# Performance work log

Measured on AMD Instinct MI355X. Metric: run time of the kernel, lower is better.

## Reference

```python
import jax, jax.numpy as jnp
import numpy as np

N_NODES = 100000
N_EDGES = 1600000
C_IN = 500
HIDDEN = 256
C_OUT = 50
K = 10
K_HALF = K // 2  # 5
ALPHA = 0.1


def _prop(x, src, dst, norm, n):
    # one propagate(): gather source features, scale by edge norm, scatter-add to dst
    msg = norm[:, None] * x[src]          # [E, F]
    return jax.ops.segment_sum(msg, dst, num_segments=n)


def setup_inputs() -> dict:
    key = jax.random.key(0)
    k0, k1, k2, k3 = jax.random.split(key, 4)
    x = jax.random.normal(k0, (N_NODES, C_IN), dtype=jnp.float32)
    edge_index = jax.random.randint(k1, (2, N_EDGES), 0, N_NODES, dtype=jnp.int32)
    # temp[k] = alpha * (1-alpha)^(2k), k = 0..K//2  (even-order PPR coefficients)
    temp = jnp.asarray(ALPHA * (1.0 - ALPHA) ** (2 * np.arange(K_HALF + 1)), dtype=jnp.float32)
    W1 = jax.random.normal(k2, (C_IN, HIDDEN), dtype=jnp.float32) / np.sqrt(C_IN).astype(np.float32)
    b1 = jnp.zeros((HIDDEN,), jnp.float32)
    W2 = jax.random.normal(k3, (HIDDEN, C_OUT), dtype=jnp.float32) / np.sqrt(HIDDEN).astype(np.float32)
    b2 = jnp.zeros((C_OUT,), jnp.float32)
    return {"x": x, "edge_index": edge_index, "W1": W1, "b1": b1, "W2": W2, "b2": b2, "temp": temp}


def reference(x, edge_index, W1, b1, W2, b2, temp):
    n = x.shape[0]
    src, dst = edge_index[0], edge_index[1]
    # sym-normalized adjacency A_hat = D^-1/2 A D^-1/2.
    # (get_laplacian 'sym' then add_self_loops(-norm, 1.0): the -1/+1 diagonal
    #  entries cancel under scatter-add, leaving exactly A_hat.)
    deg = jax.ops.segment_sum(jnp.ones_like(src, dtype=x.dtype), src, num_segments=n)
    dinv = jnp.where(deg > 0, jax.lax.rsqrt(jnp.maximum(deg, 1e-12)), 0.0)
    norm = dinv[src] * dinv[dst]          # [E]

    # MLP (dropout is identity in eval mode)
    h = jax.nn.relu(x @ W1 + b1)
    h = h @ W2 + b2                        # [N, C_OUT]

    hidden0 = h * temp[0]

    def body(k, carry):
        xk, hid = carry
        xk = _prop(xk, src, dst, norm, n)  # A_hat @ x
        xk = _prop(xk, src, dst, norm, n)  # A_hat^2 @ x
        hid = hid + temp[k + 1] * xk
        return (xk, hid)

    _, hidden = jax.lax.fori_loop(0, K_HALF, body, (h, hidden0))
    return jax.nn.log_softmax(hidden, axis=1)
```

## Files before the change

### kernel.cpp

```cpp
#include <hip/hip_runtime.h>

#define NN 100000
#define CIN 500
#define KPAD 512
#define HID 256
#define COUT 50
#define NPADOUT 64
#define FPAD 64

#define NBLK 256
#define CB 128
#define NC ((NN + CB - 1) / CB)
#define NCB (NC * NBLK)
#define NCB2 (2 * NCB)

typedef __attribute__((ext_vector_type(8))) short short8;
typedef __attribute__((ext_vector_type(4))) float f32x4;

static __device__ __forceinline__ unsigned short f2bf(float f) {
  union { float f; unsigned u; } v; v.f = f;
  unsigned r = (v.u + 0x7fffu + ((v.u >> 16) & 1u)) >> 16;
  return (unsigned short)r;
}


__launch_bounds__(256)
__global__ void k_p1(const int* __restrict__ src, const int* __restrict__ dst,
                     int* __restrict__ blk_cnt, int E, int chunk) {
  __shared__ int bd[NC], bs[NC];
  int tid = threadIdx.x;
  for (int i = tid; i < NC; i += 256) { bd[i] = 0; bs[i] = 0; }
  __syncthreads();
  int e0 = blockIdx.x * chunk, e1 = min(E, e0 + chunk);
  for (int e = e0 + tid; e < e1; e += 256) {
    atomicAdd(&bd[dst[e] >> 7], 1);
    atomicAdd(&bs[src[e] >> 7], 1);
  }
  __syncthreads();
  for (int i = tid; i < NC; i += 256) {
    blk_cnt[i * NBLK + blockIdx.x] = bd[i];
    blk_cnt[NCB + i * NBLK + blockIdx.x] = bs[i];
  }
}


__global__ void k_scan_a(const int* __restrict__ hist, int* __restrict__ incl,
                         int* __restrict__ bsum, int n) {
  __shared__ int ts[256];
  int tid = threadIdx.x;
  int base = blockIdx.x * 1024 + tid * 4;
  int a0 = 0, a1 = 0, a2 = 0, a3 = 0;
  if (base + 3 < n) {
    a0 = hist[base]; a1 = hist[base + 1]; a2 = hist[base + 2]; a3 = hist[base + 3];
  } else {
    if (base     < n) a0 = hist[base];
    if (base + 1 < n) a1 = hist[base + 1];
    if (base + 2 < n) a2 = hist[base + 2];
    if (base + 3 < n) a3 = hist[base + 3];
  }
  a1 += a0; a2 += a1; a3 += a2;
  ts[tid] = a3;
  __syncthreads();
  for (int o = 1; o < 256; o <<= 1) {
    int v = ts[tid];
    if (tid >= o) v += ts[tid - o];
    __syncthreads();
    ts[tid] = v;
    __syncthreads();
  }
  int ex = tid ? ts[tid - 1] : 0;
  if (base     < n) incl[base]     = a0 + ex;
  if (base + 1 < n) incl[base + 1] = a1 + ex;
  if (base + 2 < n) incl[base + 2] = a2 + ex;
  if (base + 3 < n) incl[base + 3] = a3 + ex;
  if (tid == 255) bsum[blockIdx.x] = ts[255];
}

__global__ void k_scan_b(const int* __restrict__ bsum, int* __restrict__ bpre, int nb) {
  __shared__ int s[512];
  int tid = threadIdx.x;
  s[tid] = (tid < nb) ? bsum[tid] : 0;
  __syncthreads();
  for (int o = 1; o < 512; o <<= 1) {
    int v = s[tid];
    if (tid >= o) v += s[tid - o];
    __syncthreads();
    s[tid] = v;
    __syncthreads();
  }
  if (tid < nb) bpre[tid] = tid ? s[tid - 1] : 0;
}

__global__ void k_scan_c(const int* __restrict__ incl, const int* __restrict__ bpre,
                         int* __restrict__ slot, int n) {
  int g = blockIdx.x * 256 + threadIdx.x;
  if (g < n) {
    slot[g + 1] = incl[g] + bpre[g >> 10];
    if (g == 0) slot[0] = 0;
  }
}


__launch_bounds__(256)
__global__ void k_p2(const int* __restrict__ src, const int* __restrict__ dst,
                     const int* __restrict__ slot, int* __restrict__ pkd,
                     unsigned char* __restrict__ pks, int E, int chunk) {
  __shared__ int cd[NC], cs[NC];
  int tid = threadIdx.x;
  for (int i = tid; i < NC; i += 256) {
    cd[i] = slot[i * NBLK + blockIdx.x];
    cs[i] = slot[NCB + i * NBLK + blockIdx.x] - E;
  }
  __syncthreads();
  int e0 = blockIdx.x * chunk, e1 = min(E, e0 + chunk);
  for (int e = e0 + tid; e < e1; e += 256) {
    int s = src[e], d = dst[e];
    int pd = atomicAdd(&cd[d >> 7], 1);
    pkd[pd] = (s << 7) | (d & 127);
    int ps = atomicAdd(&cs[s >> 7], 1);
    pks[ps] = (unsigned char)(s & 127);
  }
}


__launch_bounds__(256)
__global__ void k_p3s(const int* __restrict__ slot, const unsigned char* __restrict__ pks,
                      float* __restrict__ dinv, int E) {
  __shared__ int hist[CB];
  int b = blockIdx.x, tid = threadIdx.x;
  if (tid < CB) hist[tid] = 0;
  __syncthreads();
  int s0 = slot[NCB + b * NBLK] - E;
  int s1 = slot[NCB + (b + 1) * NBLK] - E;
  for (int e = s0 + tid; e < s1; e += 256) atomicAdd(&hist[pks[e]], 1);
  __syncthreads();
  if (tid < CB) {
    int node = b * CB + tid;
    if (node < NN) {
      int c = hist[tid];
      dinv[node] = c > 0 ? rsqrtf((float)c) : 0.f;
    }
  }
}


__launch_bounds__(256)
__global__ void k_p3d(const int* __restrict__ slot, const int* __restrict__ pkd,
                      const float* __restrict__ dinv, int* __restrict__ offs,
                      int2* __restrict__ epk, int E) {
  __shared__ int hist[CB], base[CB], cur[CB];
  int b = blockIdx.x, tid = threadIdx.x;
  if (tid < CB) hist[tid] = 0;
  __syncthreads();
  int s0 = slot[b * NBLK];
  int s1 = slot[(b + 1) * NBLK];
  for (int e = s0 + tid; e < s1; e += 256) atomicAdd(&hist[pkd[e] & 127], 1);
  __syncthreads();
  if (tid == 0) {
    int acc = s0;
    for (int i = 0; i < CB; i++) { base[i] = acc; cur[i] = acc; acc += hist[i]; }
  }
  __syncthreads();
  if (tid < CB) {
    int node = b * CB + tid;
    if (node < NN) offs[node] = base[tid];
  }
  if (b == gridDim.x - 1 && tid == 0) offs[NN] = E;
  for (int e = s0 + tid; e < s1; e += 256) {
    int pk = pkd[e];
    int fine = pk & 127, s = pk >> 7;
    int pos = atomicAdd(&cur[fine], 1);
    float nm = dinv[s] * dinv[b * CB + fine];
    epk[pos] = make_int2(s, __float_as_int(nm));
  }
}


__global__ void k_wt(const float* __restrict__ W1, const float* __restrict__ W2,
                     unsigned short* __restrict__ W1T, unsigned short* __restrict__ W2T) {
  int idx = blockIdx.x * 256 + threadIdx.x;
  if (idx < HID * KPAD) {
    int n = idx >> 9, k = idx & 511;
    W1T[idx] = (k < CIN) ? f2bf(W1[(long)k * HID + n]) : (unsigned short)0;
  } else if (idx < HID * KPAD + NPADOUT * HID) {
    int i2 = idx - HID * KPAD;
    int n = i2 >> 8, k = i2 & 255;
    W2T[i2] = (n < COUT) ? f2bf(W2[(long)k * COUT + n]) : (unsigned short)0;
  }
}


__launch_bounds__(512)
__global__ void k_gemm1(const float* __restrict__ X, const unsigned short* __restrict__ W1T,
                        const float* __restrict__ b1, unsigned short* __restrict__ HB) {
  __shared__ unsigned short As[128 * 40];
  __shared__ unsigned short Bs[256 * 40];
  const int tid = threadIdx.x;
  const int lane = tid & 63, w = tid >> 6;
  const int wr = w >> 2, wc = w & 3;
  const int row0 = blockIdx.x * 128;
  f32x4 acc[4][4] = {};
  const int sr = tid >> 3, sc = tid & 7;
  const int br = tid >> 2, bc = tid & 3;

  float4 ra[2];
  uint4 rb[2];
#pragma unroll
  for (int p = 0; p < 2; p++) {
    int grow = row0 + sr + p * 64;
    int gr = grow < NN ? grow : NN - 1;
    float4 f = *reinterpret_cast<const float4*>(&X[(long)gr * CIN + sc * 4]);
    if (grow >= NN) { f.x = 0.f; f.y = 0.f; f.z = 0.f; f.w = 0.f; }
    ra[p] = f;
    rb[p] = *reinterpret_cast<const uint4*>(&W1T[(long)(br + p * 128) * KPAD + bc * 8]);
  }

  for (int ks = 0; ks < 16; ks++) {
    const int kk = ks * 32;
#pragma unroll
    for (int p = 0; p < 2; p++) {
      ushort4 val;
      val.x = f2bf(ra[p].x); val.y = f2bf(ra[p].y);
      val.z = f2bf(ra[p].z); val.w = f2bf(ra[p].w);
      *reinterpret_cast<ushort4*>(&As[(sr + p * 64) * 40 + sc * 4]) = val;
      *reinterpret_cast<uint4*>(&Bs[(br + p * 128) * 40 + bc * 8]) = rb[p];
    }
    if (ks < 15) {
      const int nk = kk + 32;
      const int gk = nk + sc * 4;
      const bool kok = gk < CIN;
      const int gkc = kok ? gk : 0;
#pragma unroll
      for (int p = 0; p < 2; p++) {
        int grow = row0 + sr + p * 64;
        int gr = grow < NN ? grow : NN - 1;
        float4 f = *reinterpret_cast<const float4*>(&X[(long)gr * CIN + gkc]);
        if (grow >= NN || !kok) { f.x = 0.f; f.y = 0.f; f.z = 0.f; f.w = 0.f; }
        ra[p] = f;
        rb[p] = *reinterpret_cast<const uint4*>(&W1T[(long)(br + p * 128) * KPAD + nk + bc * 8]);
      }
    }
    __syncthreads();
    short8 af[4], bfr[4];
    const int koff = (lane >> 4) * 8;
#pragma unroll
    for (int i = 0; i < 4; i++)
      af[i] = *reinterpret_cast<const short8*>(&As[(wr * 64 + i * 16 + (lane & 15)) * 40 + koff]);
#pragma unroll
    for (int j = 0; j < 4; j++)
      bfr[j] = *reinterpret_cast<const short8*>(&Bs[(wc * 64 + j * 16 + (lane & 15)) * 40 + koff]);
#pragma unroll
    for (int i = 0; i < 4; i++)
#pragma unroll
      for (int j = 0; j < 4; j++)
        acc[i][j] = __builtin_amdgcn_mfma_f32_16x16x32_bf16(af[i], bfr[j], acc[i][j], 0, 0, 0);
    __syncthreads();
  }
#pragma unroll
  for (int i = 0; i < 4; i++) {
    int rbase = row0 + wr * 64 + i * 16 + (lane >> 4) * 4;
#pragma unroll
    for (int j = 0; j < 4; j++) {
      int col = wc * 64 + j * 16 + (lane & 15);
      float bv = b1[col];
#pragma unroll
      for (int r = 0; r < 4; r++) {
        int row = rbase + r;
        if (row < NN) {
          float v = acc[i][j][r] + bv;
          v = v > 0.f ? v : 0.f;
          HB[(long)row * HID + col] = f2bf(v);
        }
      }
    }
  }
}


__launch_bounds__(256)
__global__ void k_gemm2(const unsigned short* __restrict__ HB, const unsigned short* __restrict__ W2T,
                        const float* __restrict__ b2, const float* __restrict__ temp,
                        unsigned short* __restrict__ X0B, float* __restrict__ HIDB) {
  __shared__ unsigned short As[128 * 40];
  __shared__ unsigned short Bs[64 * 40];
  const int tid = threadIdx.x;
  const int lane = tid & 63, w = tid >> 6;
  const int row0 = blockIdx.x * 128;
  f32x4 acc[2][4] = {};
  const int ar = tid >> 2, ac = tid & 3;

  for (int kk = 0; kk < HID; kk += 32) {
    __syncthreads();
#pragma unroll
    for (int p = 0; p < 2; p++) {
      int r = ar + p * 64;
      int grow = row0 + r;
      uint4 v;
      if (grow < NN) v = *reinterpret_cast<const uint4*>(&HB[(long)grow * HID + kk + ac * 8]);
      else { v.x = v.y = v.z = v.w = 0; }
      *reinterpret_cast<uint4*>(&As[r * 40 + ac * 8]) = v;
    }
    {
      int nl = tid >> 2, c = tid & 3;
      const uint4 v = *reinterpret_cast<const uint4*>(&W2T[nl * HID + kk + c * 8]);
      *reinterpret_cast<uint4*>(&Bs[nl * 40 + c * 8]) = v;
    }
    __syncthreads();
    short8 af[2], bfr[4];
    const int koff = (lane >> 4) * 8;
#pragma unroll
    for (int i = 0; i < 2; i++)
      af[i] = *reinterpret_cast<const short8*>(&As[(w * 32 + i * 16 + (lane & 15)) * 40 + koff]);
#pragma unroll
    for (int j = 0; j < 4; j++)
      bfr[j] = *reinterpret_cast<const short8*>(&Bs[(j * 16 + (lane & 15)) * 40 + koff]);
#pragma unroll
    for (int i = 0; i < 2; i++)
#pragma unroll
      for (int j = 0; j < 4; j++)
        acc[i][j] = __builtin_amdgcn_mfma_f32_16x16x32_bf16(af[i], bfr[j], acc[i][j], 0, 0, 0);
  }
  float t0 = temp[0];
#pragma unroll
  for (int i = 0; i < 2; i++) {
    int rbase = row0 + w * 32 + i * 16 + (lane >> 4) * 4;
#pragma unroll
    for (int j = 0; j < 4; j++) {
      int col = j * 16 + (lane & 15);
      if (col < COUT) {
        float bv = b2[col];
#pragma unroll
        for (int r = 0; r < 4; r++) {
          int row = rbase + r;
          if (row < NN) {
            float v = acc[i][j][r] + bv;
            X0B[((long)row << 6) + col] = f2bf(v);
            HIDB[(long)row * COUT + col] = t0 * v;
          }
        }
      }
    }
  }
}


__launch_bounds__(256)
__global__ void k_prop(const int* __restrict__ offs, const int2* __restrict__ epk,
                       const unsigned short* __restrict__ xin,
                       unsigned short* __restrict__ xout, float* __restrict__ hid,
                       const float* __restrict__ temp, int accidx) {
  int node = blockIdx.x * 8 + (threadIdx.x >> 5);
  if (node >= NN) return;
  int h = threadIdx.x & 31;
  int fp = h * 2;
  int s0 = offs[node], s1 = offs[node + 1];
  float a0 = 0.f, a1 = 0.f;
  int e = s0;
  for (; e + 3 < s1; e += 4) {
    int2 p0 = epk[e], p1 = epk[e + 1], p2 = epk[e + 2], p3 = epk[e + 3];
    unsigned v0 = *reinterpret_cast<const unsigned*>(&xin[((long)p0.x << 6) + fp]);
    unsigned v1 = *reinterpret_cast<const unsigned*>(&xin[((long)p1.x << 6) + fp]);
    unsigned v2 = *reinterpret_cast<const unsigned*>(&xin[((long)p2.x << 6) + fp]);
    unsigned v3 = *reinterpret_cast<const unsigned*>(&xin[((long)p3.x << 6) + fp]);
    float w0 = __int_as_float(p0.y), w1 = __int_as_float(p1.y);
    float w2 = __int_as_float(p2.y), w3 = __int_as_float(p3.y);
    a0 += w0 * __uint_as_float(v0 << 16) + w1 * __uint_as_float(v1 << 16)
        + w2 * __uint_as_float(v2 << 16) + w3 * __uint_as_float(v3 << 16);
    a1 += w0 * __uint_as_float(v0 & 0xffff0000u) + w1 * __uint_as_float(v1 & 0xffff0000u)
        + w2 * __uint_as_float(v2 & 0xffff0000u) + w3 * __uint_as_float(v3 & 0xffff0000u);
  }
  for (; e < s1; e++) {
    int2 p0 = epk[e];
    float w0 = __int_as_float(p0.y);
    unsigned v0 = *reinterpret_cast<const unsigned*>(&xin[((long)p0.x << 6) + fp]);
    a0 += w0 * __uint_as_float(v0 << 16);
    a1 += w0 * __uint_as_float(v0 & 0xffff0000u);
  }
  if (fp < COUT) {
    unsigned pk = ((unsigned)f2bf(a1) << 16) | (unsigned)f2bf(a0);
    *reinterpret_cast<unsigned*>(&xout[((long)node << 6) + fp]) = pk;
    if (accidx >= 0) {
      float t = temp[accidx];
      float2* hp = reinterpret_cast<float2*>(&hid[(long)node * COUT + fp]);
      float2 o = *hp;
      o.x += t * a0; o.y += t * a1;
      *hp = o;
    }
  }
}


__launch_bounds__(256)
__global__ void k_lsm(const float* __restrict__ hid, float* __restrict__ out) {
  int node = blockIdx.x * 4 + (threadIdx.x >> 6);
  if (node >= NN) return;
  int f = threadIdx.x & 63;
  float v = (f < COUT) ? hid[(long)node * COUT + f] : -INFINITY;
  float m = v;
#pragma unroll
  for (int o = 32; o > 0; o >>= 1) m = fmaxf(m, __shfl_xor(m, o, 64));
  float ex = (f < COUT) ? expf(v - m) : 0.f;
  float s = ex;
#pragma unroll
  for (int o = 32; o > 0; o >>= 1) s += __shfl_xor(s, o, 64);
  if (f < COUT) out[(long)node * COUT + f] = (v - m) - logf(s);
}


extern "C" void kernel_launch(void* const* d_in, const int* in_sizes, int n_in,
                              void* d_out, int out_size, void* d_ws, size_t ws_size,
                              hipStream_t stream) {
  const float* X  = (const float*)d_in[0];
  const int* EI   = (const int*)d_in[1];
  const float* W1 = (const float*)d_in[2];
  const float* B1 = (const float*)d_in[3];
  const float* W2 = (const float*)d_in[4];
  const float* B2 = (const float*)d_in[5];
  const float* TEMP = (const float*)d_in[6];
  const int E = in_sizes[1] / 2;
  const int* src = EI;
  const int* dst = EI + E;

  char* ws = (char*)d_ws;
  size_t off = 0;
  auto alloc = [&](size_t bytes) -> void* {
    off = (off + 511) & ~(size_t)511;
    void* p = ws + off;
    off += bytes;
    return p;
  };
  unsigned short* HB  = (unsigned short*)alloc((size_t)NN * HID * 2);
  unsigned short* W1T = (unsigned short*)alloc((size_t)HID * KPAD * 2);
  unsigned short* W2T = (unsigned short*)alloc((size_t)NPADOUT * HID * 2);
  unsigned short* X0B = (unsigned short*)alloc((size_t)NN * FPAD * 2);
  unsigned short* X1B = (unsigned short*)alloc((size_t)NN * FPAD * 2);
  float* HIDB = (float*)alloc((size_t)NN * COUT * 4);
  float* DINV = (float*)alloc((size_t)NN * 4);
  int* OFFS   = (int*)alloc((size_t)(NN + 1) * 4);
  int* BLKC   = (int*)alloc((size_t)NCB2 * 4);
  int* INCL   = (int*)alloc((size_t)NCB2 * 4);
  int* SLOT   = (int*)alloc((size_t)(NCB2 + 1) * 4);
  int* BSUM   = (int*)alloc(512 * 4);
  int* BPRE   = (int*)alloc(512 * 4);
  int* PKD    = (int*)alloc((size_t)E * 4);
  unsigned char* PKS = (unsigned char*)alloc((size_t)E);
  int2* EPK   = (int2*)alloc((size_t)E * 8);

  const int chunk = (E + NBLK - 1) / NBLK;
  const int nscan = NCB2;
  const int nsa = (nscan + 1023) / 1024;

  k_p1<<<NBLK, 256, 0, stream>>>(src, dst, BLKC, E, chunk);
  k_scan_a<<<nsa, 256, 0, stream>>>(BLKC, INCL, BSUM, nscan);
  k_scan_b<<<1, 512, 0, stream>>>(BSUM, BPRE, nsa);
  k_scan_c<<<(nscan + 255) / 256, 256, 0, stream>>>(INCL, BPRE, SLOT, nscan);
  k_p2<<<NBLK, 256, 0, stream>>>(src, dst, SLOT, PKD, PKS, E, chunk);
  k_p3s<<<NC, 256, 0, stream>>>(SLOT, PKS, DINV, E);
  k_p3d<<<NC, 256, 0, stream>>>(SLOT, PKD, DINV, OFFS, EPK, E);

  k_wt<<<(HID * KPAD + NPADOUT * HID + 255) / 256, 256, 0, stream>>>(W1, W2, W1T, W2T);

  k_gemm1<<<(NN + 127) / 128, 512, 0, stream>>>(X, W1T, B1, HB);
  k_gemm2<<<(NN + 127) / 128, 256, 0, stream>>>(HB, W2T, B2, TEMP, X0B, HIDB);

  const int PB = (NN + 7) / 8;
  for (int k = 0; k < 5; k++) {
    k_prop<<<PB, 256, 0, stream>>>(OFFS, EPK, X0B, X1B, HIDB, TEMP, -1);
    k_prop<<<PB, 256, 0, stream>>>(OFFS, EPK, X1B, X0B, HIDB, TEMP, k + 1);
  }
  k_lsm<<<(NN + 3) / 4, 256, 0, stream>>>(HIDB, (float*)d_out);
}
```

Baseline: 974.1 us.

## Fuse MLP GEMMs, drop scan_c kernel, unroll propagate gather by eight

Merges the two MLP GEMMs into one kernel that keeps the ReLU hidden tile in shared memory and runs the second GEMM from it, so the bf16 hidden matrix is never written to or re-read from global memory. Removes the separate slot-materialisation scan kernel by computing slot offsets on the fly from the inclusive scan and block prefixes. Adds an 8-wide unrolled gather loop in propagation to keep more loads in flight. In exchange, the first GEMM loses its register prefetch of the next K-tile, and the fused kernel adds extra barriers and a larger shared-memory footprint, which may lower occupancy.

```diff
diff --git a/kernel.cpp b/kernel.cpp
--- a/kernel.cpp
+++ b/kernel.cpp
@@ -21,6 +21,11 @@
   union { float f; unsigned u; } v; v.f = f;
   unsigned r = (v.u + 0x7fffu + ((v.u >> 16) & 1u)) >> 16;
   return (unsigned short)r;
+}
+
+static __device__ __forceinline__ int slotAt(const int* __restrict__ incl,
+                                             const int* __restrict__ bpre, int g) {
+  return g ? incl[g - 1] + bpre[(g - 1) >> 10] : 0;
 }
 
 
@@ -91,25 +96,16 @@
   if (tid < nb) bpre[tid] = tid ? s[tid - 1] : 0;
 }
 
-__global__ void k_scan_c(const int* __restrict__ incl, const int* __restrict__ bpre,
-                         int* __restrict__ slot, int n) {
-  int g = blockIdx.x * 256 + threadIdx.x;
-  if (g < n) {
-    slot[g + 1] = incl[g] + bpre[g >> 10];
-    if (g == 0) slot[0] = 0;
-  }
-}
-
 
 __launch_bounds__(256)
 __global__ void k_p2(const int* __restrict__ src, const int* __restrict__ dst,
-                     const int* __restrict__ slot, int* __restrict__ pkd,
-                     unsigned char* __restrict__ pks, int E, int chunk) {
+                     const int* __restrict__ incl, const int* __restrict__ bpre,
+                     int* __restrict__ pkd, unsigned char* __restrict__ pks, int E, int chunk) {
   __shared__ int cd[NC], cs[NC];
   int tid = threadIdx.x;
   for (int i = tid; i < NC; i += 256) {
-    cd[i] = slot[i * NBLK + blockIdx.x];
-    cs[i] = slot[NCB + i * NBLK + blockIdx.x] - E;
+    cd[i] = slotAt(incl, bpre, i * NBLK + blockIdx.x);
+    cs[i] = slotAt(incl, bpre, NCB + i * NBLK + blockIdx.x) - E;
   }
   __syncthreads();
   int e0 = blockIdx.x * chunk, e1 = min(E, e0 + chunk);
@@ -124,14 +120,14 @@
 
 
 __launch_bounds__(256)
-__global__ void k_p3s(const int* __restrict__ slot, const unsigned char* __restrict__ pks,
-                      float* __restrict__ dinv, int E) {
+__global__ void k_p3s(const int* __restrict__ incl, const int* __restrict__ bpre,
+                      const unsigned char* __restrict__ pks, float* __restrict__ dinv, int E) {
   __shared__ int hist[CB];
   int b = blockIdx.x, tid = threadIdx.x;
   if (tid < CB) hist[tid] = 0;
   __syncthreads();
-  int s0 = slot[NCB + b * NBLK] - E;
-  int s1 = slot[NCB + (b + 1) * NBLK] - E;
+  int s0 = slotAt(incl, bpre, NCB + b * NBLK) - E;
+  int s1 = slotAt(incl, bpre, NCB + (b + 1) * NBLK) - E;
   for (int e = s0 + tid; e < s1; e += 256) atomicAdd(&hist[pks[e]], 1);
   __syncthreads();
   if (tid < CB) {
@@ -145,15 +141,15 @@
 
 
 __launch_bounds__(256)
-__global__ void k_p3d(const int* __restrict__ slot, const int* __restrict__ pkd,
-                      const float* __restrict__ dinv, int* __restrict__ offs,
-                      int2* __restrict__ epk, int E) {
+__global__ void k_p3d(const int* __restrict__ incl, const int* __restrict__ bpre,
+                      const int* __restrict__ pkd, const float* __restrict__ dinv,
+                      int* __restrict__ offs, int2* __restrict__ epk, int E) {
   __shared__ int hist[CB], base[CB], cur[CB];
   int b = blockIdx.x, tid = threadIdx.x;
   if (tid < CB) hist[tid] = 0;
   __syncthreads();
-  int s0 = slot[b * NBLK];
-  int s1 = slot[(b + 1) * NBLK];
+  int s0 = slotAt(incl, bpre, b * NBLK);
+  int s1 = slotAt(incl, bpre, (b + 1) * NBLK);
   for (int e = s0 + tid; e < s1; e += 256) atomicAdd(&hist[pkd[e] & 127], 1);
   __syncthreads();
   if (tid == 0) {
@@ -191,10 +187,13 @@
 
 
 __launch_bounds__(512)
-__global__ void k_gemm1(const float* __restrict__ X, const unsigned short* __restrict__ W1T,
-                        const float* __restrict__ b1, unsigned short* __restrict__ HB) {
-  __shared__ unsigned short As[128 * 40];
-  __shared__ unsigned short Bs[256 * 40];
+__global__ void k_mlp(const float* __restrict__ X, const unsigned short* __restrict__ W1T,
+                      const float* __restrict__ b1, const unsigned short* __restrict__ W2T,
+                      const float* __restrict__ b2, const float* __restrict__ temp,
+                      unsigned short* __restrict__ X0B, float* __restrict__ HIDB) {
+  __shared__ unsigned short smem[64 * 264];
+  unsigned short* As = smem;
+  unsigned short* Bs = smem + 128 * 40;
   const int tid = threadIdx.x;
   const int lane = tid & 63, w = tid >> 6;
   const int wr = w >> 2, wc = w & 3;
@@ -203,42 +202,27 @@
   const int sr = tid >> 3, sc = tid & 7;
   const int br = tid >> 2, bc = tid & 3;
 
-  float4 ra[2];
-  uint4 rb[2];
-#pragma unroll
-  for (int p = 0; p < 2; p++) {
-    int grow = row0 + sr + p * 64;
-    int gr = grow < NN ? grow : NN - 1;
-    float4 f = *reinterpret_cast<const float4*>(&X[(long)gr * CIN + sc * 4]);
-    if (grow >= NN) { f.x = 0.f; f.y = 0.f; f.z = 0.f; f.w = 0.f; }
-    ra[p] = f;
-    rb[p] = *reinterpret_cast<const uint4*>(&W1T[(long)(br + p * 128) * KPAD + bc * 8]);
-  }
-
-  for (int ks = 0; ks < 16; ks++) {
-    const int kk = ks * 32;
+  for (int kk = 0; kk < KPAD; kk += 32) {
+    __syncthreads();
 #pragma unroll
     for (int p = 0; p < 2; p++) {
+      int r = sr + p * 64;
+      int grow = row0 + r;
+      int gk = kk + sc * 4;
       ushort4 val;
-      val.x = f2bf(ra[p].x); val.y = f2bf(ra[p].y);
-      val.z = f2bf(ra[p].z); val.w = f2bf(ra[p].w);
-      *reinterpret_cast<ushort4*>(&As[(sr + p * 64) * 40 + sc * 4]) = val;
-      *reinterpret_cast<uint4*>(&Bs[(br + p * 128) * 40 + bc * 8]) = rb[p];
-    }
-    if (ks < 15) {
-      const int nk = kk + 32;
-      const int gk = nk + sc * 4;
-      const bool kok = gk < CIN;
-      const int gkc = kok ? gk : 0;
-#pragma unroll
-      for (int p = 0; p < 2; p++) {
-        int grow = row0 + sr + p * 64;
-        int gr = grow < NN ? grow : NN - 1;
-        float4 f = *reinterpret_cast<const float4*>(&X[(long)gr * CIN + gkc]);
-        if (grow >= NN || !kok) { f.x = 0.f; f.y = 0.f; f.z = 0.f; f.w = 0.f; }
-        ra[p] = f;
-        rb[p] = *reinterpret_cast<const uint4*>(&W1T[(long)(br + p * 128) * KPAD + nk + bc * 8]);
+      if (grow < NN && gk < CIN) {
+        const float4 f = *reinterpret_cast<const float4*>(&X[(long)grow * CIN + gk]);
+        val.x = f2bf(f.x); val.y = f2bf(f.y); val.z = f2bf(f.z); val.w = f2bf(f.w);
+      } else {
+        val.x = val.y = val.z = val.w = 0;
       }
+      *reinterpret_cast<ushort4*>(&As[r * 40 + sc * 4]) = val;
+    }
+#pragma unroll
+    for (int p = 0; p < 2; p++) {
+      int nl = br + p * 128;
+      const uint4 v = *reinterpret_cast<const uint4*>(&W1T[(long)nl * KPAD + kk + bc * 8]);
+      *reinterpret_cast<uint4*>(&Bs[nl * 40 + bc * 8]) = v;
     }
     __syncthreads();
     short8 af[4], bfr[4];
@@ -254,89 +238,55 @@
 #pragma unroll
       for (int j = 0; j < 4; j++)
         acc[i][j] = __builtin_amdgcn_mfma_f32_16x16x32_bf16(af[i], bfr[j], acc[i][j], 0, 0, 0);
-    __syncthreads();
-  }
-#pragma unroll
-  for (int i = 0; i < 4; i++) {
-    int rbase = row0 + wr * 64 + i * 16 + (lane >> 4) * 4;
-#pragma unroll
-    for (int j = 0; j < 4; j++) {
-      int col = wc * 64 + j * 16 + (lane & 15);
-      float bv = b1[col];
-#pragma unroll
-      for (int r = 0; r < 4; r++) {
-        int row = rbase + r;
-        if (row < NN) {
-          float v = acc[i][j][r] + bv;
-          v = v > 0.f ? v : 0.f;
-          HB[(long)row * HID + col] = f2bf(v);
+  }
+
+  unsigned short* Hs = smem;
+  const float t0 = temp[0];
+  const int rt = w >> 1;
+  const int jh = w & 1;
+#pragma unroll
+  for (int ph = 0; ph < 2; ph++) {
+    __syncthreads();
+    if (wr == ph) {
+#pragma unroll
+      for (int i = 0; i < 4; i++) {
+        int lr = i * 16 + (lane >> 4) * 4;
+#pragma unroll
+        for (int j = 0; j < 4; j++) {
+          int col = wc * 64 + j * 16 + (lane & 15);
+          float bv = b1[col];
+#pragma unroll
+          for (int r = 0; r < 4; r++) {
+            float v = acc[i][j][r] + bv;
+            v = v > 0.f ? v : 0.f;
+            Hs[(lr + r) * 264 + col] = f2bf(v);
+          }
         }
       }
     }
-  }
-}
-
-
-__launch_bounds__(256)
-__global__ void k_gemm2(const unsigned short* __restrict__ HB, const unsigned short* __restrict__ W2T,
-                        const float* __restrict__ b2, const float* __restrict__ temp,
-                        unsigned short* __restrict__ X0B, float* __restrict__ HIDB) {
-  __shared__ unsigned short As[128 * 40];
-  __shared__ unsigned short Bs[64 * 40];
-  const int tid = threadIdx.x;
-  const int lane = tid & 63, w = tid >> 6;
-  const int row0 = blockIdx.x * 128;
-  f32x4 acc[2][4] = {};
-  const int ar = tid >> 2, ac = tid & 3;
-
-  for (int kk = 0; kk < HID; kk += 32) {
-    __syncthreads();
-#pragma unroll
-    for (int p = 0; p < 2; p++) {
-      int r = ar + p * 64;
-      int grow = row0 + r;
-      uint4 v;
-      if (grow < NN) v = *reinterpret_cast<const uint4*>(&HB[(long)grow * HID + kk + ac * 8]);
-      else { v.x = v.y = v.z = v.w = 0; }
-      *reinterpret_cast<uint4*>(&As[r * 40 + ac * 8]) = v;
-    }
-    {
-      int nl = tid >> 2, c = tid & 3;
-      const uint4 v = *reinterpret_cast<const uint4*>(&W2T[nl * HID + kk + c * 8]);
-      *reinterpret_cast<uint4*>(&Bs[nl * 40 + c * 8]) = v;
-    }
-    __syncthreads();
-    short8 af[2], bfr[4];
+    __syncthreads();
+    f32x4 acc2[2] = {};
     const int koff = (lane >> 4) * 8;
-#pragma unroll
-    for (int i = 0; i < 2; i++)
-      af[i] = *reinterpret_cast<const short8*>(&As[(w * 32 + i * 16 + (lane & 15)) * 40 + koff]);
-#pragma unroll
-    for (int j = 0; j < 4; j++)
-      bfr[j] = *reinterpret_cast<const short8*>(&Bs[(j * 16 + (lane & 15)) * 40 + koff]);
-#pragma unroll
-    for (int i = 0; i < 2; i++)
-#pragma unroll
-      for (int j = 0; j < 4; j++)
-        acc[i][j] = __builtin_amdgcn_mfma_f32_16x16x32_bf16(af[i], bfr[j], acc[i][j], 0, 0, 0);
-  }
-  float t0 = temp[0];
-#pragma unroll
-  for (int i = 0; i < 2; i++) {
-    int rbase = row0 + w * 32 + i * 16 + (lane >> 4) * 4;
-#pragma unroll
-    for (int j = 0; j < 4; j++) {
-      int col = j * 16 + (lane & 15);
-      if (col < COUT) {
-        float bv = b2[col];
-#pragma unroll
-        for (int r = 0; r < 4; r++) {
-          int row = rbase + r;
-          if (row < NN) {
-            float v = acc[i][j][r] + bv;
-            X0B[((long)row << 6) + col] = f2bf(v);
-            HIDB[(long)row * COUT + col] = t0 * v;
-          }
+    for (int kk = 0; kk < HID; kk += 32) {
+      short8 a = *reinterpret_cast<const short8*>(&Hs[(rt * 16 + (lane & 15)) * 264 + kk + koff]);
+#pragma unroll
+      for (int jj = 0; jj < 2; jj++) {
+        int n = (jh * 2 + jj) * 16 + (lane & 15);
+        short8 b = *reinterpret_cast<const short8*>(&W2T[n * HID + kk + koff]);
+        acc2[jj] = __builtin_amdgcn_mfma_f32_16x16x32_bf16(a, b, acc2[jj], 0, 0, 0);
+      }
+    }
+#pragma unroll
+    for (int jj = 0; jj < 2; jj++) {
+      int col = (jh * 2 + jj) * 16 + (lane & 15);
+      float bv = (col < COUT) ? b2[col] : 0.f;
+#pragma unroll
+      for (int r = 0; r < 4; r++) {
+        int row = row0 + ph * 64 + rt * 16 + (lane >> 4) * 4 + r;
+        if (row < NN) {
+          float v = acc2[jj][r] + bv;
+          X0B[((long)row << 6) + col] = f2bf(v);
+          if (col < COUT) HIDB[(long)row * COUT + col] = t0 * v;
         }
       }
     }
@@ -356,6 +306,21 @@
   int s0 = offs[node], s1 = offs[node + 1];
   float a0 = 0.f, a1 = 0.f;
   int e = s0;
+  for (; e + 7 < s1; e += 8) {
+    int2 p[8];
+#pragma unroll
+    for (int q = 0; q < 8; q++) p[q] = epk[e + q];
+    unsigned v[8];
+#pragma unroll
+    for (int q = 0; q < 8; q++)
+      v[q] = *reinterpret_cast<const unsigned*>(&xin[((long)p[q].x << 6) + fp]);
+#pragma unroll
+    for (int q = 0; q < 8; q++) {
+      float wq = __int_as_float(p[q].y);
+      a0 += wq * __uint_as_float(v[q] << 16);
+      a1 += wq * __uint_as_float(v[q] & 0xffff0000u);
+    }
+  }
   for (; e + 3 < s1; e += 4) {
     int2 p0 = epk[e], p1 = epk[e + 1], p2 = epk[e + 2], p3 = epk[e + 3];
     unsigned v0 = *reinterpret_cast<const unsigned*>(&xin[((long)p0.x << 6) + fp]);
@@ -429,7 +394,6 @@
     off += bytes;
     return p;
   };
-  unsigned short* HB  = (unsigned short*)alloc((size_t)NN * HID * 2);
   unsigned short* W1T = (unsigned short*)alloc((size_t)HID * KPAD * 2);
   unsigned short* W2T = (unsigned short*)alloc((size_t)NPADOUT * HID * 2);
   unsigned short* X0B = (unsigned short*)alloc((size_t)NN * FPAD * 2);
@@ -439,7 +403,6 @@
   int* OFFS   = (int*)alloc((size_t)(NN + 1) * 4);
   int* BLKC   = (int*)alloc((size_t)NCB2 * 4);
   int* INCL   = (int*)alloc((size_t)NCB2 * 4);
-  int* SLOT   = (int*)alloc((size_t)(NCB2 + 1) * 4);
   int* BSUM   = (int*)alloc(512 * 4);
   int* BPRE   = (int*)alloc(512 * 4);
   int* PKD    = (int*)alloc((size_t)E * 4);
@@ -447,21 +410,18 @@
   int2* EPK   = (int2*)alloc((size_t)E * 8);
 
   const int chunk = (E + NBLK - 1) / NBLK;
-  const int nscan = NCB2;
-  const int nsa = (nscan + 1023) / 1024;
+  const int nsa = (NCB2 + 1023) / 1024;
 
   k_p1<<<NBLK, 256, 0, stream>>>(src, dst, BLKC, E, chunk);
-  k_scan_a<<<nsa, 256, 0, stream>>>(BLKC, INCL, BSUM, nscan);
+  k_scan_a<<<nsa, 256, 0, stream>>>(BLKC, INCL, BSUM, NCB2);
   k_scan_b<<<1, 512, 0, stream>>>(BSUM, BPRE, nsa);
-  k_scan_c<<<(nscan + 255) / 256, 256, 0, stream>>>(INCL, BPRE, SLOT, nscan);
-  k_p2<<<NBLK, 256, 0, stream>>>(src, dst, SLOT, PKD, PKS, E, chunk);
-  k_p3s<<<NC, 256, 0, stream>>>(SLOT, PKS, DINV, E);
-  k_p3d<<<NC, 256, 0, stream>>>(SLOT, PKD, DINV, OFFS, EPK, E);
+  k_p2<<<NBLK, 256, 0, stream>>>(src, dst, INCL, BPRE, PKD, PKS, E, chunk);
+  k_p3s<<<NC, 256, 0, stream>>>(INCL, BPRE, PKS, DINV, E);
+  k_p3d<<<NC, 256, 0, stream>>>(INCL, BPRE, PKD, DINV, OFFS, EPK, E);
 
   k_wt<<<(HID * KPAD + NPADOUT * HID + 255) / 256, 256, 0, stream>>>(W1, W2, W1T, W2T);
 
-  k_gemm1<<<(NN + 127) / 128, 512, 0, stream>>>(X, W1T, B1, HB);
-  k_gemm2<<<(NN + 127) / 128, 256, 0, stream>>>(HB, W2T, B2, TEMP, X0B, HIDB);
+  k_mlp<<<(NN + 127) / 128, 512, 0, stream>>>(X, W1T, B1, W2T, B2, TEMP, X0B, HIDB);
 
   const int PB = (NN + 7) / 8;
   for (int k = 0; k < 5; k++) {
```

New measurement: 906.7 us. 1.07x faster.
